# Optimization experiments

Measured on AMD Instinct MI355X. Metric: run time of the kernel, lower is better.

Reference implementation:

```python
import jax, jax.numpy as jnp
import numpy as np

NB_STEPS = 50  # quadrature steps (51 Clenshaw-Curtis nodes)
IN_D = 8
HIDDEN = [256, 256, 256]
B = 8192


def _cc_quadrature(nb_steps):
    # Clenshaw-Curtis weights/nodes, exactly as in UMNN's ParallelNeuralIntegral
    lam = np.arange(nb_steps + 1).reshape(-1, 1)
    lam = np.cos((lam @ lam.T) * np.pi / nb_steps)
    lam[:, 0] = 0.5
    lam[:, -1] = 0.5 * lam[:, -1]
    lam = lam * 2.0 / nb_steps
    W = np.arange(nb_steps + 1).reshape(-1, 1)
    W[np.arange(1, nb_steps + 1, 2)] = 0
    W = 2.0 / (1 - W.astype(np.float64) ** 2)
    W[0] = 1.0
    W[np.arange(1, nb_steps + 1, 2)] = 0.0
    cc_weights = (lam.T @ W).astype(np.float32)  # [S+1, 1]
    steps = np.cos(np.arange(nb_steps + 1).reshape(-1, 1) * np.pi / nb_steps).astype(np.float32)  # [S+1,1]
    return jnp.asarray(cc_weights), jnp.asarray(steps)


def setup_inputs() -> dict:
    key = jax.random.key(0)
    ks = jax.random.split(key, 20)
    inp = {
        "x": jax.random.normal(ks[0], (B, 1), dtype=jnp.float32),
        "h": jax.random.normal(ks[1], (B, IN_D - 1), dtype=jnp.float32),
    }
    # integrand net: in_d -> 256 -> 256 -> 256 -> 1
    i_dims = [IN_D] + HIDDEN + [1]
    for li, (d0, d1) in enumerate(zip(i_dims, i_dims[1:])):
        scale = 1.0 / np.sqrt(d0)
        inp[f"iW{li}"] = jax.random.uniform(ks[2 + li], (d0, d1), jnp.float32, -scale, scale)
        inp[f"ib{li}"] = jax.random.uniform(ks[6 + li], (d1,), jnp.float32, -scale, scale)
    # h net: (in_d-1) -> 256 -> 256 -> 256 -> 2
    h_dims = [IN_D - 1] + HIDDEN + [2]
    for li, (d0, d1) in enumerate(zip(h_dims, h_dims[1:])):
        scale = 1.0 / np.sqrt(d0)
        inp[f"hW{li}"] = jax.random.uniform(ks[10 + li], (d0, d1), jnp.float32, -scale, scale)
        inp[f"hb{li}"] = jax.random.uniform(ks[14 + li], (d1,), jnp.float32, -scale, scale)
    return inp


def _integrand(z, Ws, bs):
    # IntegrandNN: Linear+ReLU chain, final Linear+ELU, then +1
    for W, b in zip(Ws[:-1], bs[:-1]):
        z = jax.nn.relu(z @ W + b)
    return jax.nn.elu(z @ Ws[-1] + bs[-1]) + 1.0


def _hnet(z, Ws, bs):
    # Linear+ReLU chain, final Linear (ReLU popped)
    for W, b in zip(Ws[:-1], bs[:-1]):
        z = jax.nn.relu(z @ W + b)
    return z @ Ws[-1] + bs[-1]


def _forward(x, h, iWs, ibs, hWs, hbs):
    cc_w, steps = _cc_quadrature(NB_STEPS)  # [S,1], [S,1]
    S = NB_STEPS + 1
    b = x.shape[0]
    # quadrature nodes mapped from [-1,1] to [0, x] (x0 = 0)
    X = x[:, None, :] * (steps[None, :, :] + 1.0) * 0.5          # [B,S,1]
    Hs = jnp.broadcast_to(h[:, None, :], (b, S, h.shape[1]))     # [B,S,in_d-1]
    z = jnp.concatenate([X, Hs], axis=-1)                        # [B,S,in_d]
    dz = _integrand(z, iWs, ibs)                                 # [B,S,1]
    integral = jnp.sum(dz * cc_w[None, :, :], axis=1) * x * 0.5  # [B,1]
    out = _hnet(h, hWs, hbs)                                     # [B,2]
    offset = out[:, :1]
    scaling = jnp.exp(out[:, 1:2])
    return scaling * integral + offset


def reference(x, h, iW0, ib0, iW1, ib1, iW2, ib2, iW3, ib3,
              hW0, hb0, hW1, hb1, hW2, hb2, hW3, hb3):
    iWs = [iW0, iW1, iW2, iW3]
    ibs = [ib0, ib1, ib2, ib3]
    hWs = [hW0, hW1, hW2, hW3]
    hbs = [hb0, hb1, hb2, hb3]
    return _forward(x, h, iWs, ibs, hWs, hbs)
```

## Files before the change

### kernel.cpp

```cpp
#include <hip/hip_runtime.h>
#include <hip/hip_bf16.h>
#include <math.h>

using bf16x8 = __attribute__((ext_vector_type(8))) __bf16;
using f32x4  = __attribute__((ext_vector_type(4))) float;

#define B_SZ    8192
#define S_STEPS 51
#define M_ROWS  (B_SZ * S_STEPS)

__device__ __forceinline__ f32x4 mfma16(bf16x8 a, bf16x8 b, f32x4 c) {
    return __builtin_amdgcn_mfma_f32_16x16x32_bf16(a, b, c, 0, 0, 0);
}

__global__ void ccq_kernel(float* __restrict__ ccw, float* __restrict__ stp) {
    int s = threadIdx.x;
    if (s >= S_STEPS) return;
    double pi50 = M_PI / 50.0;
    double acc = 0.0;
    for (int j = 0; j <= 50; j += 2) {
        double wq = (j == 0) ? 1.0 : 2.0 / (1.0 - (double)(j * j));
        double m;
        if (s == 0) m = 0.5;
        else if (s == 50) m = 0.5;
        else m = cos((double)(j * s) * pi50);
        acc += m * wq;
    }
    ccw[s] = (float)(acc * (2.0 / 50.0));
    stp[s] = (float)cos((double)s * pi50);
}

struct PackArgs {
    const float* src[8];
    __hip_bfloat16* dst[8];
    int Ks[8], Ns[8], KST[8];
    int prefix[9];
};

__global__ void pack_all(PackArgs pa) {
    int idx = blockIdx.x * 256 + threadIdx.x;
    if (idx >= pa.prefix[8]) return;
    int m = 0;
    while (idx >= pa.prefix[m + 1]) ++m;
    int e = idx - pa.prefix[m];
    int KSTEPS = pa.KST[m];
    int j    = e & 7;
    int lane = (e >> 3) & 63;
    int ks   = (e >> 9) % KSTEPS;
    int cg   = (e >> 9) / KSTEPS;
    int col = cg * 16 + (lane & 15);
    int k   = ks * 32 + (lane >> 4) * 8 + j;
    float v = (k < pa.Ks[m] && col < pa.Ns[m]) ? pa.src[m][k * pa.Ns[m] + col] : 0.0f;
    ((__bf16*)pa.dst[m])[e] = (__bf16)v;
}


template<int KSTEPS, int CHUNKS, int MASK, int NF>
__device__ __forceinline__ void gemm_layer(const __bf16* __restrict__ actIn,
                                           const __bf16* __restrict__ wpack,
                                           const float* __restrict__ bias,
                                           __bf16* __restrict__ actOut,
                                           int wid, int lane) {
    const bf16x8* wp = (const bf16x8*)wpack;
    f32x4 acc[4][NF];
#pragma unroll
    for (int m = 0; m < 4; ++m)
#pragma unroll
        for (int n = 0; n < NF; ++n) acc[m][n] = (f32x4)0.0f;

    for (int ks = 0; ks < KSTEPS; ++ks) {
        bf16x8 af[4];
#pragma unroll
        for (int m = 0; m < 4; ++m) {
            int row   = m * 16 + (lane & 15);
            int chunk = ks * 4 + (lane >> 4);
            int idx16 = row * CHUNKS + (chunk ^ (row & MASK));
            af[m] = *(const bf16x8*)(actIn + idx16 * 8);
        }
        bf16x8 bf[NF];
#pragma unroll
        for (int n = 0; n < NF; ++n) {
            int cg = wid * NF + n;
            bf[n] = wp[(cg * KSTEPS + ks) * 64 + lane];
        }
#pragma unroll
        for (int m = 0; m < 4; ++m)
#pragma unroll
            for (int n = 0; n < NF; ++n)
                acc[m][n] = mfma16(af[m], bf[n], acc[m][n]);
    }
#pragma unroll
    for (int n = 0; n < NF; ++n) {
        int col = (wid * NF + n) * 16 + (lane & 15);
        float bv = bias[col];
#pragma unroll
        for (int m = 0; m < 4; ++m) {
#pragma unroll
            for (int r = 0; r < 4; ++r) {
                float v = acc[m][n][r] + bv;
                v = fmaxf(v, 0.0f);
                int row = m * 16 + (lane >> 4) * 4 + r;
                int idx = (row * 32 + ((col >> 3) ^ (row & 7))) * 8 + (col & 7);
                actOut[idx] = (__bf16)v;
            }
        }
    }
}

template<int MODE>
__device__ __forceinline__ void final_layer(const __bf16* __restrict__ actIn,
                                            const __bf16* __restrict__ wpack,
                                            const float* __restrict__ bias,
                                            float* __restrict__ out0,
                                            float* __restrict__ out1,
                                            int rb, int wid, int lane) {
    const bf16x8* wp = (const bf16x8*)wpack;
    f32x4 acc = (f32x4)0.0f;
    for (int ks = 0; ks < 8; ++ks) {
        int row   = wid * 16 + (lane & 15);
        int chunk = ks * 4 + (lane >> 4);
        bf16x8 af = *(const bf16x8*)(actIn + (row * 32 + (chunk ^ (row & 7))) * 8);
        acc = mfma16(af, wp[ks * 64 + lane], acc);
    }
    int col = lane & 15;
    if (MODE == 0) {
        if (col == 0) {
            float b = bias[0];
#pragma unroll
            for (int r = 0; r < 4; ++r) {
                int row = wid * 16 + (lane >> 4) * 4 + r;
                float v = acc[r] + b;
                out0[rb + row] = (v > 0.0f) ? (v + 1.0f) : expf(v);
            }
        }
    } else {
        if (col < 2) {
            float b = bias[col];
            float* dst = (col == 0) ? out0 : out1;
#pragma unroll
            for (int r = 0; r < 4; ++r) {
                int row = wid * 16 + (lane >> 4) * 4 + r;
                dst[rb + row] = acc[r] + b;
            }
        }
    }
}

template<int MODE>
__global__ __launch_bounds__(512, 4) void mlp_kernel(
    const float* __restrict__ x, const float* __restrict__ h,
    const float* __restrict__ steps,
    const __bf16* __restrict__ w0p, const __bf16* __restrict__ w1p,
    const __bf16* __restrict__ w2p, const __bf16* __restrict__ w3p,
    const float* __restrict__ b0, const float* __restrict__ b1,
    const float* __restrict__ b2, const float* __restrict__ b3,
    float* __restrict__ out0, float* __restrict__ out1) {
    __shared__ __bf16 actA[64 * 256];
    __shared__ __bf16 actB[64 * 256];
    __bf16* zin = actB;

    int tid  = threadIdx.x;
    int lane = tid & 63;
    int wid  = tid >> 6;
    int rb   = blockIdx.x * 64;

    if (tid < 256) {
        int row   = tid >> 2;
        int cpart = tid & 3;
        float vals[8];
        if (MODE == 0) {
            int s  = rb >> 13;
            int i  = (rb & (B_SZ - 1)) + row;
            float sc = (steps[s] + 1.0f) * 0.5f;
#pragma unroll
            for (int j = 0; j < 8; ++j) {
                int c = cpart * 8 + j;
                float v = 0.0f;
                if (c == 0) v = x[i] * sc;
                else if (c < 8) v = h[i * 7 + c - 1];
                vals[j] = v;
            }
        } else {
            int i = rb + row;
#pragma unroll
            for (int j = 0; j < 8; ++j) {
                int c = cpart * 8 + j;
                vals[j] = (c < 7) ? h[i * 7 + c] : 0.0f;
            }
        }
        bf16x8 zv;
#pragma unroll
        for (int j = 0; j < 8; ++j) zv[j] = (__bf16)vals[j];
        int zidx = (row * 4 + (cpart ^ (row & 3))) * 8;
        *(bf16x8*)(zin + zidx) = zv;
    }
    __syncthreads();

    gemm_layer<1, 4, 3, 2>(zin, w0p, b0, actA, wid, lane);
    __syncthreads();
    gemm_layer<8, 32, 7, 2>(actA, w1p, b1, actB, wid, lane);
    __syncthreads();
    gemm_layer<8, 32, 7, 2>(actB, w2p, b2, actA, wid, lane);
    __syncthreads();
    if (wid < 4)
        final_layer<MODE>(actA, w3p, b3, out0, out1, rb, wid, lane);
}

__global__ void reduce_kernel(const float* __restrict__ dz, const float* __restrict__ x,
                              const float* __restrict__ ho, const float* __restrict__ hs,
                              const float* __restrict__ ccw, float* __restrict__ out) {
    __shared__ float w[S_STEPS];
    int t = threadIdx.x;
    if (t < S_STEPS) w[t] = ccw[t];
    __syncthreads();
    int i = blockIdx.x * blockDim.x + t;
    float acc = 0.0f;
    for (int s = 0; s < S_STEPS; ++s) acc += dz[s * B_SZ + i] * w[s];
    float integral = acc * x[i] * 0.5f;
    out[i] = expf(hs[i]) * integral + ho[i];
}

extern "C" void kernel_launch(void* const* d_in, const int* in_sizes, int n_in,
                              void* d_out, int out_size, void* d_ws, size_t ws_size,
                              hipStream_t stream) {
    (void)in_sizes; (void)n_in; (void)out_size; (void)ws_size;
    const float* x = (const float*)d_in[0];
    const float* h = (const float*)d_in[1];
    const float* iW[4] = {(const float*)d_in[2], (const float*)d_in[4],
                          (const float*)d_in[6], (const float*)d_in[8]};
    const float* ib[4] = {(const float*)d_in[3], (const float*)d_in[5],
                          (const float*)d_in[7], (const float*)d_in[9]};
    const float* hW[4] = {(const float*)d_in[10], (const float*)d_in[12],
                          (const float*)d_in[14], (const float*)d_in[16]};
    const float* hb[4] = {(const float*)d_in[11], (const float*)d_in[13],
                          (const float*)d_in[15], (const float*)d_in[17]};

    size_t off = 0;
    auto alloc = [&](size_t bytes) -> void* {
        void* p = (char*)d_ws + off;
        off += (bytes + 255) & ~(size_t)255;
        return p;
    };
    float*  dz   = (float*)alloc((size_t)M_ROWS * 4);
    float*  ho   = (float*)alloc(B_SZ * 4);
    float*  hs   = (float*)alloc(B_SZ * 4);
    float*  ccw  = (float*)alloc(64 * 4);
    float*  stp  = (float*)alloc(64 * 4);
    __bf16* iW0p = (__bf16*)alloc(16 * 1 * 512 * 2);
    __bf16* iW1p = (__bf16*)alloc(16 * 8 * 512 * 2);
    __bf16* iW2p = (__bf16*)alloc(16 * 8 * 512 * 2);
    __bf16* iW3p = (__bf16*)alloc(1 * 8 * 512 * 2);
    __bf16* hW0p = (__bf16*)alloc(16 * 1 * 512 * 2);
    __bf16* hW1p = (__bf16*)alloc(16 * 8 * 512 * 2);
    __bf16* hW2p = (__bf16*)alloc(16 * 8 * 512 * 2);
    __bf16* hW3p = (__bf16*)alloc(1 * 8 * 512 * 2);

    ccq_kernel<<<1, 64, 0, stream>>>(ccw, stp);

    PackArgs pa;
    const float* srcs[8] = {iW[0], iW[1], iW[2], iW[3], hW[0], hW[1], hW[2], hW[3]};
    __bf16*      dsts[8] = {iW0p, iW1p, iW2p, iW3p, hW0p, hW1p, hW2p, hW3p};
    int Ks[8]  = {8, 256, 256, 256, 7, 256, 256, 256};
    int Ns[8]  = {256, 256, 256, 1, 256, 256, 256, 2};
    int KST[8] = {1, 8, 8, 8, 1, 8, 8, 8};
    int CG[8]  = {16, 16, 16, 1, 16, 16, 16, 1};
    int pfx = 0;
    for (int m = 0; m < 8; ++m) {
        pa.src[m] = srcs[m];
        pa.dst[m] = (__hip_bfloat16*)dsts[m];
        pa.Ks[m] = Ks[m]; pa.Ns[m] = Ns[m]; pa.KST[m] = KST[m];
        pa.prefix[m] = pfx;
        pfx += CG[m] * KST[m] * 512;
    }
    pa.prefix[8] = pfx;
    pack_all<<<(pfx + 255) / 256, 256, 0, stream>>>(pa);

    mlp_kernel<0><<<M_ROWS / 64, 512, 0, stream>>>(
        x, h, stp, iW0p, iW1p, iW2p, iW3p, ib[0], ib[1], ib[2], ib[3], dz, dz);
    mlp_kernel<1><<<B_SZ / 64, 512, 0, stream>>>(
        x, h, stp, hW0p, hW1p, hW2p, hW3p, hb[0], hb[1], hb[2], hb[3], ho, hs);

    reduce_kernel<<<B_SZ / 256, 256, 0, stream>>>(dz, x, ho, hs, ccw, (float*)d_out);
}
```

Before: 153.3 us.

## Retile MLP GEMM warps to 16x128 tiles with B-fragment double buffering

Each of the 8 waves now computes a 16-row by 128-column tile (wave row and column split) instead of 64 rows by 32 columns. Weight fragments are double-buffered across k-steps, and the epilogue writes packed bf16 pairs as 32-bit stores. To make those packed stores line up, the activation feature order is permuted, and the packed weight rows of the later layers are permuted to match. This cuts LDS A-loads and narrow LDS stores but raises global weight traffic per wave and register pressure. The occupancy hint in launch bounds is also dropped.

New measurement: 264.7 us. 72.7% more time.

```diff
diff --git a/kernel.cpp b/kernel.cpp
--- a/kernel.cpp
+++ b/kernel.cpp
@@ -33,7 +33,7 @@
 struct PackArgs {
     const float* src[8];
     __hip_bfloat16* dst[8];
-    int Ks[8], Ns[8], KST[8];
+    int Ks[8], Ns[8], KST[8], perm[8];
     int prefix[9];
 };
 
@@ -50,59 +50,57 @@
     int cg   = (e >> 9) / KSTEPS;
     int col = cg * 16 + (lane & 15);
     int k   = ks * 32 + (lane >> 4) * 8 + j;
-    float v = (k < pa.Ks[m] && col < pa.Ns[m]) ? pa.src[m][k * pa.Ns[m] + col] : 0.0f;
+    int kk  = pa.perm[m] ? ((k & ~31) + ((k & 31) >> 1) + (k & 1) * 16) : k;
+    float v = (kk < pa.Ks[m] && col < pa.Ns[m]) ? pa.src[m][kk * pa.Ns[m] + col] : 0.0f;
     ((__bf16*)pa.dst[m])[e] = (__bf16)v;
 }
 
 
-template<int KSTEPS, int CHUNKS, int MASK, int NF>
+template<int KSTEPS, int CHUNKS, int MASK>
 __device__ __forceinline__ void gemm_layer(const __bf16* __restrict__ actIn,
                                            const __bf16* __restrict__ wpack,
                                            const float* __restrict__ bias,
                                            __bf16* __restrict__ actOut,
-                                           int wid, int lane) {
+                                           int wr, int wc, int lane) {
     const bf16x8* wp = (const bf16x8*)wpack;
-    f32x4 acc[4][NF];
-#pragma unroll
-    for (int m = 0; m < 4; ++m)
-#pragma unroll
-        for (int n = 0; n < NF; ++n) acc[m][n] = (f32x4)0.0f;
-
+    const int la = lane & 15, hi = lane >> 4;
+    f32x4 acc[8];
+#pragma unroll
+    for (int n = 0; n < 8; ++n) acc[n] = (f32x4)0.0f;
+
+    bf16x8 bbuf[2][8];
+#pragma unroll
+    for (int n = 0; n < 8; ++n)
+        bbuf[0][n] = wp[((wc * 8 + n) * KSTEPS) * 64 + lane];
+
+#pragma unroll
     for (int ks = 0; ks < KSTEPS; ++ks) {
-        bf16x8 af[4];
-#pragma unroll
-        for (int m = 0; m < 4; ++m) {
-            int row   = m * 16 + (lane & 15);
-            int chunk = ks * 4 + (lane >> 4);
-            int idx16 = row * CHUNKS + (chunk ^ (row & MASK));
-            af[m] = *(const bf16x8*)(actIn + idx16 * 8);
-        }
-        bf16x8 bf[NF];
-#pragma unroll
-        for (int n = 0; n < NF; ++n) {
-            int cg = wid * NF + n;
-            bf[n] = wp[(cg * KSTEPS + ks) * 64 + lane];
-        }
-#pragma unroll
-        for (int m = 0; m < 4; ++m)
-#pragma unroll
-            for (int n = 0; n < NF; ++n)
-                acc[m][n] = mfma16(af[m], bf[n], acc[m][n]);
-    }
-#pragma unroll
-    for (int n = 0; n < NF; ++n) {
-        int col = (wid * NF + n) * 16 + (lane & 15);
-        float bv = bias[col];
-#pragma unroll
-        for (int m = 0; m < 4; ++m) {
-#pragma unroll
-            for (int r = 0; r < 4; ++r) {
-                float v = acc[m][n][r] + bv;
-                v = fmaxf(v, 0.0f);
-                int row = m * 16 + (lane >> 4) * 4 + r;
-                int idx = (row * 32 + ((col >> 3) ^ (row & 7))) * 8 + (col & 7);
-                actOut[idx] = (__bf16)v;
-            }
+        int row   = wr * 16 + la;
+        int chunk = ks * 4 + hi;
+        bf16x8 af = *(const bf16x8*)(actIn + (row * CHUNKS + (chunk ^ (row & MASK))) * 8);
+        if (ks + 1 < KSTEPS) {
+#pragma unroll
+            for (int n = 0; n < 8; ++n)
+                bbuf[(ks + 1) & 1][n] = wp[((wc * 8 + n) * KSTEPS + ks + 1) * 64 + lane];
+        }
+#pragma unroll
+        for (int n = 0; n < 8; ++n)
+            acc[n] = mfma16(af, bbuf[ks & 1][n], acc[n]);
+    }
+#pragma unroll
+    for (int p = 0; p < 4; ++p) {
+        int f0 = wc * 128 + p * 32 + la;
+        float b0 = bias[f0], b1 = bias[f0 + 16];
+        int kd = wc * 64 + p * 16 + la;
+        unsigned* dst = (unsigned*)actOut;
+#pragma unroll
+        for (int r = 0; r < 4; ++r) {
+            int row = wr * 16 + hi * 4 + r;
+            float v0 = fmaxf(acc[2 * p][r] + b0, 0.0f);
+            float v1 = fmaxf(acc[2 * p + 1][r] + b1, 0.0f);
+            union { __bf16 h[2]; unsigned u; } cv;
+            cv.h[0] = (__bf16)v0; cv.h[1] = (__bf16)v1;
+            dst[(row * 32 + ((kd >> 2) ^ (row & 7))) * 4 + (kd & 3)] = cv.u;
         }
     }
 }
@@ -147,7 +145,7 @@
 }
 
 template<int MODE>
-__global__ __launch_bounds__(512, 4) void mlp_kernel(
+__global__ __launch_bounds__(512) void mlp_kernel(
     const float* __restrict__ x, const float* __restrict__ h,
     const float* __restrict__ steps,
     const __bf16* __restrict__ w0p, const __bf16* __restrict__ w1p,
@@ -162,6 +160,8 @@
     int tid  = threadIdx.x;
     int lane = tid & 63;
     int wid  = tid >> 6;
+    int wr   = wid >> 1;
+    int wc   = wid & 1;
     int rb   = blockIdx.x * 64;
 
     if (tid < 256) {
@@ -196,11 +196,11 @@
     }
     __syncthreads();
 
-    gemm_layer<1, 4, 3, 2>(zin, w0p, b0, actA, wid, lane);
-    __syncthreads();
-    gemm_layer<8, 32, 7, 2>(actA, w1p, b1, actB, wid, lane);
-    __syncthreads();
-    gemm_layer<8, 32, 7, 2>(actB, w2p, b2, actA, wid, lane);
+    gemm_layer<1, 4, 3>(zin, w0p, b0, actA, wr, wc, lane);
+    __syncthreads();
+    gemm_layer<8, 32, 7>(actA, w1p, b1, actB, wr, wc, lane);
+    __syncthreads();
+    gemm_layer<8, 32, 7>(actB, w2p, b2, actA, wr, wc, lane);
     __syncthreads();
     if (wid < 4)
         final_layer<MODE>(actA, w3p, b3, out0, out1, rb, wid, lane);
@@ -264,11 +264,12 @@
     int Ns[8]  = {256, 256, 256, 1, 256, 256, 256, 2};
     int KST[8] = {1, 8, 8, 8, 1, 8, 8, 8};
     int CG[8]  = {16, 16, 16, 1, 16, 16, 16, 1};
+    int PM[8]  = {0, 1, 1, 1, 0, 1, 1, 1};
     int pfx = 0;
     for (int m = 0; m < 8; ++m) {
         pa.src[m] = srcs[m];
         pa.dst[m] = (__hip_bfloat16*)dsts[m];
-        pa.Ks[m] = Ks[m]; pa.Ns[m] = Ns[m]; pa.KST[m] = KST[m];
+        pa.Ks[m] = Ks[m]; pa.Ns[m] = Ns[m]; pa.KST[m] = KST[m]; pa.perm[m] = PM[m];
         pa.prefix[m] = pfx;
         pfx += CG[m] * KST[m] * 512;
     }
```
